# Kernel tuning notes

Measured on AMD Instinct MI355X. Metric: run time of the kernel, lower is better.

## Reference

```python
import jax, jax.numpy as jnp
import numpy as np

B, S, D, H = 8, 512, 2048, 16
DOWN, UP, R = 512, 2048, 512
HD = D // H        # 128, used only in the additive scale
VHD = UP // H      # 128, content head dim / value head dim
BASE = 10000.0


def _rope_tables(head_dim):
    # Faithful to source: positions span arange(head_dim), NOT max_len.
    pos = jnp.arange(head_dim, dtype=jnp.float32)
    div = jnp.exp(jnp.arange(0, head_dim, 2, dtype=jnp.float32) * (-np.log(BASE) / head_dim))
    theta = jnp.outer(pos, div)          # [head_dim, head_dim//2]
    return jnp.sin(theta), jnp.cos(theta)


def _apply_rope(q, num_heads, head_dim):
    # q: [B, S, num_heads*head_dim] -> [B, num_heads, S, head_dim] with interleaved rotation
    b, s, _ = q.shape
    q = q.reshape(b, s, num_heads, head_dim).transpose(0, 2, 1, 3)
    sin, cos = _rope_tables(head_dim)
    sin = sin[:s][None, None]            # [1,1,S,head_dim//2]
    cos = cos[:s][None, None]
    q_ = q.reshape(b, num_heads, s, head_dim // 2, 2)
    q1, q2 = q_[..., 0], q_[..., 1]
    o1 = q1 * cos - q2 * sin
    o2 = q2 * cos + q1 * sin
    return jnp.stack([o1, o2], axis=-1).reshape(b, num_heads, s, head_dim)


def setup_inputs() -> dict:
    key = jax.random.key(0)
    ks = jax.random.split(key, 18)
    w = lambda k, shp: jax.random.normal(k, shp, jnp.float32) * 0.02
    return {
        "X":    jax.random.normal(ks[0], (B, S, D), jnp.float32),
        "Wdq":  w(ks[1], (D, DOWN)),      "bdq":  w(ks[2], (DOWN,)),
        "Wdkv": w(ks[3], (D, DOWN)),      "bdkv": w(ks[4], (DOWN,)),
        "Wuq":  w(ks[5], (DOWN, UP)),     "buq":  w(ks[6], (UP,)),
        "Wuk":  w(ks[7], (DOWN, UP)),     "buk":  w(ks[8], (UP,)),
        "Wuv":  w(ks[9], (DOWN, UP)),     "buv":  w(ks[10], (UP,)),
        "Wqr":  w(ks[11], (DOWN, R * H)), "bqr":  w(ks[12], (R * H,)),
        "Wkr":  w(ks[13], (D, R)),        "bkr":  w(ks[14], (R,)),
        "Wfc":  w(ks[15], (VHD * H, D)),  "bfc":  w(ks[16], (D,)),
    }


def reference(X, Wdq, bdq, Wdkv, bdkv, Wuq, buq, Wuk, buk, Wuv, buv,
              Wqr, bqr, Wkr, bkr, Wfc, bfc):
    b, s, _ = X.shape
    c_q = X @ Wdq + bdq                                  # [B,S,DOWN]
    c_kv = X @ Wdkv + bdkv                               # [B,S,DOWN]
    q_c = (c_q @ Wuq + buq).reshape(b, s, H, VHD).transpose(0, 2, 1, 3)   # [B,H,S,VHD]
    k_c = (c_kv @ Wuk + buk).reshape(b, s, H, VHD).transpose(0, 2, 1, 3)
    v_c = (c_kv @ Wuv + buv).reshape(b, s, H, VHD).transpose(0, 2, 1, 3)
    q_r = _apply_rope(c_q @ Wqr + bqr, H, R)             # [B,H,S,R]
    k_r = _apply_rope(X @ Wkr + bkr, 1, R)               # [B,1,S,R]
    q = jnp.concatenate([q_c, q_r], axis=-1)             # [B,H,S,VHD+R]
    k = jnp.concatenate([k_c, jnp.broadcast_to(k_r, (b, H, s, R))], axis=-1)
    scale = HD ** 0.5 + R ** 0.5                         # additive scale, as in source
    scores = jnp.einsum('bhqd,bhkd->bhqk', q, k) / scale
    attn = jax.nn.softmax(scores, axis=-1)               # dropout: eval mode (identity)
    o = jnp.einsum('bhqk,bhkd->bhqd', attn, v_c).transpose(0, 2, 1, 3).reshape(b, s, H * VHD)
    return o @ Wfc + bfc
```

## Files before the change

### kernel.cpp

```cpp
#include <hip/hip_runtime.h>
#include <hip/hip_bf16.h>
#include <stdint.h>

typedef unsigned short u16;
typedef short bf16x8 __attribute__((ext_vector_type(8)));
typedef float f32x4 __attribute__((ext_vector_type(4)));

__device__ __forceinline__ float us2f(u16 u) {
    union { unsigned int i; float f; } x;
    x.i = ((unsigned int)u) << 16;
    return x.f;
}

__device__ __forceinline__ u16 f2us(float f) {
    union { float f; unsigned int i; } x; x.f = f;
    unsigned int lsb = (x.i >> 16) & 1u;
    x.i += 0x7FFFu + lsb;
    return (u16)(x.i >> 16);
}

__device__ __forceinline__ void gl_lds16(const u16* g, u16* l) {
    __builtin_amdgcn_global_load_lds(
        (const __attribute__((address_space(1))) void*)(uintptr_t)(const void*)g,
        (__attribute__((address_space(3))) void*)(uintptr_t)(void*)l,
        16, 0, 0);
}

#define FLAG_ROPE2  1
#define FLAG_SCALE  2
#define FLAG_TRANS2 4
#define FLAG_F32OUT 8

struct GArgs {
    const u16 *A0, *B0, *B0r2, *A1, *B1;
    long sA0o, sA0i, sB0o, sB0i, sA1o, sA1i, sB1o, sB1i;
    int K0, K1;
    const float* bias;
    void* C; void* C2; long sCo, sCi;
    int colSplit;
    int innerCnt;
    float scale;
};

template <int LDA0, int LDB0, int LDC, int LDC2, int FLAGS, int LDA1, int LDB1>
__global__ __launch_bounds__(256)
void gemm_mfma(GArgs g)
{
    __shared__ u16 As[128 * 64];
    __shared__ u16 Bs[128 * 64];

    const int t    = threadIdx.x;
    const int lane = t & 63;
    const int w    = t >> 6;
    const int wm   = w >> 1, wn = w & 1;
    const int m0   = blockIdx.y * 128;
    const int n0   = blockIdx.x * 128;
    const bool r2  = (n0 >= g.colSplit);

    const int z  = blockIdx.z;
    const int zo = z / g.innerCnt, zi = z - zo * g.innerCnt;

    const int srow = t >> 3;
    const int sp   = t & 7;
    u16* dA = As + t * 8;
    u16* dB = Bs + t * 8;

    const int lr = lane & 15;
    const int jj = lane >> 4;

    f32x4 acc[4][4];
#pragma unroll
    for (int i = 0; i < 4; ++i)
#pragma unroll
        for (int j = 0; j < 4; ++j)
            acc[i][j] = (f32x4){0.f, 0.f, 0.f, 0.f};

    auto mfma_tile = [&]() {
#pragma unroll
        for (int s = 0; s < 2; ++s) {
            bf16x8 af[4], bfr[4];
#pragma unroll
            for (int mi = 0; mi < 4; ++mi) {
                int row  = wm * 64 + mi * 16 + lr;
                int slot = (s * 4 + jj + row) & 7;
                af[mi] = *(const bf16x8*)&As[row * 64 + slot * 8];
            }
#pragma unroll
            for (int ni = 0; ni < 4; ++ni) {
                int row  = wn * 64 + ni * 16 + lr;
                int slot = (s * 4 + jj + row) & 7;
                bfr[ni] = *(const bf16x8*)&Bs[row * 64 + slot * 8];
            }
#pragma unroll
            for (int mi = 0; mi < 4; ++mi)
#pragma unroll
                for (int ni = 0; ni < 4; ++ni)
                    acc[mi][ni] = __builtin_amdgcn_mfma_f32_16x16x32_bf16(
                        af[mi], bfr[ni], acc[mi][ni], 0, 0, 0);
        }
    };

    {
        const u16* A = g.A0 + zo * g.sA0o + zi * g.sA0i;
        const u16* B = (r2 ? g.B0r2 - (long)g.colSplit * LDB0 : g.B0)
                       + zo * g.sB0o + zi * g.sB0i;
        const u16* gA[4];
        const u16* gB[4];
#pragma unroll
        for (int r = 0; r < 4; ++r) {
            int row = r * 32 + srow;
            int gc  = (sp - row) & 7;
            gA[r] = A + (long)(m0 + row) * LDA0 + gc * 8;
            gB[r] = B + (long)(n0 + row) * LDB0 + gc * 8;
        }
        for (int kt = 0; kt < g.K0; kt += 64) {
#pragma unroll
            for (int r = 0; r < 4; ++r) {
                gl_lds16(gA[r], dA + r * 2048);
                gl_lds16(gB[r], dB + r * 2048);
                gA[r] += 64; gB[r] += 64;
            }
            __syncthreads();
            mfma_tile();
            __syncthreads();
        }
    }

    if (LDA1 != 0) {
        const u16* A = g.A1 + zo * g.sA1o + zi * g.sA1i;
        const u16* B = g.B1 + zo * g.sB1o + zi * g.sB1i;
        const u16* gA[4];
        const u16* gB[4];
#pragma unroll
        for (int r = 0; r < 4; ++r) {
            int row = r * 32 + srow;
            int gc  = (sp - row) & 7;
            gA[r] = A + (long)(m0 + row) * (LDA1 ? LDA1 : 1) + gc * 8;
            gB[r] = B + (long)(n0 + row) * (LDB1 ? LDB1 : 1) + gc * 8;
        }
        for (int kt = 0; kt < g.K1; kt += 64) {
#pragma unroll
            for (int r = 0; r < 4; ++r) {
                gl_lds16(gA[r], dA + r * 2048);
                gl_lds16(gB[r], dB + r * 2048);
                gA[r] += 64; gB[r] += 64;
            }
            __syncthreads();
            mfma_tile();
            __syncthreads();
        }
    }

    const int eCol0 = n0 + wn * 64 + lr;
    const int eRow0 = m0 + wm * 64 + jj * 4;
    const bool oddc = lane & 1;

    float biasv[4];
    if (g.bias) {
#pragma unroll
        for (int ni = 0; ni < 4; ++ni) biasv[ni] = g.bias[eCol0 + ni * 16];
    }

#pragma unroll
    for (int mi = 0; mi < 4; ++mi) {
#pragma unroll
        for (int ni = 0; ni < 4; ++ni) {
            f32x4 v = acc[mi][ni];
            if (g.bias) {
                float bv = biasv[ni];
                v[0] += bv; v[1] += bv; v[2] += bv; v[3] += bv;
            }
            if (FLAGS & FLAG_SCALE) {
                v[0] *= g.scale; v[1] *= g.scale; v[2] *= g.scale; v[3] *= g.scale;
            }
            const int colg = eCol0 + ni * 16;
            const int rowb = eRow0 + mi * 16;
            if (!r2) {
                if (FLAGS & FLAG_F32OUT) {
                    float* cp = (float*)g.C + zo * g.sCo + zi * g.sCi;
#pragma unroll
                    for (int i = 0; i < 4; ++i)
                        cp[(long)(rowb + i) * LDC + colg] = v[i];
                } else {
                    u16* cp = (u16*)g.C + zo * g.sCo + zi * g.sCi;
#pragma unroll
                    for (int i = 0; i < 4; ++i)
                        cp[(long)(rowb + i) * LDC + colg] = f2us(v[i]);
                }
            } else {
                const int col2 = colg - g.colSplit;
                if (FLAGS & FLAG_ROPE2) {
                    int rp = col2 & 511 & ~1;
                    float freq = __expf(-9.2103403719761836f * (float)rp * (1.0f / 512.0f));
#pragma unroll
                    for (int i = 0; i < 4; ++i) {
                        float th = (float)((rowb + i) & 511) * freq;
                        float sn, cs;
                        __sincosf(th, &sn, &cs);
                        float other = __shfl_xor(v[i], 1, 64);
                        v[i] = oddc ? (v[i] * cs + other * sn)
                                    : (v[i] * cs - other * sn);
                    }
                }
                if (FLAGS & FLAG_TRANS2) {
                    u16* cp = (u16*)g.C2 + (long)col2 * LDC2 + rowb;
                    ushort4 o4;
                    o4.x = f2us(v[0]); o4.y = f2us(v[1]);
                    o4.z = f2us(v[2]); o4.w = f2us(v[3]);
                    *(ushort4*)cp = o4;
                } else {
                    u16* cp = (u16*)g.C2;
#pragma unroll
                    for (int i = 0; i < 4; ++i)
                        cp[(long)(rowb + i) * LDC2 + col2] = f2us(v[i]);
                }
            }
        }
    }
}

__global__ __launch_bounds__(256)
void pv_soft(const u16* __restrict__ attn, const u16* __restrict__ v_t,
             u16* __restrict__ o, int b0)
{
    __shared__ u16 Ae[32 * 512];
    __shared__ u16 Bv[128 * 64];
    __shared__ float l_arr[32];

    const int t    = threadIdx.x;
    const int lane = t & 63;
    const int w    = t >> 6;
    const int z    = blockIdx.y;
    const int bb   = b0 + (z >> 4);
    const int h    = z & 15;
    const int m0   = blockIdx.x * 32;

    const u16* Abase = attn + (long)z * 262144 + (long)m0 * 512;
#pragma unroll
    for (int i = 0; i < 8; ++i) {
        int row = w * 8 + i;
        int gc  = (lane - row) & 63;
        gl_lds16(Abase + (long)row * 512 + gc * 8, Ae + row * 512 + lane * 8);
    }
    __syncthreads();

    {
        int r = t >> 3, p = t & 7;
        u16* rp_ = Ae + r * 512;
        float mx = -1e30f;
#pragma unroll
        for (int j = 0; j < 8; ++j) {
            int slot = (p + 8 * j + r) & 63;
            bf16x8 vv = *(const bf16x8*)&rp_[slot * 8];
#pragma unroll
            for (int e = 0; e < 8; ++e) mx = fmaxf(mx, us2f(((u16*)&vv)[e]));
        }
        mx = fmaxf(mx, __shfl_xor(mx, 1, 64));
        mx = fmaxf(mx, __shfl_xor(mx, 2, 64));
        mx = fmaxf(mx, __shfl_xor(mx, 4, 64));
        float s = 0.f;
#pragma unroll
        for (int j = 0; j < 8; ++j) {
            int slot = (p + 8 * j + r) & 63;
            bf16x8 vv = *(const bf16x8*)&rp_[slot * 8];
            bf16x8 ov;
#pragma unroll
            for (int e = 0; e < 8; ++e) {
                float ee = __expf(us2f(((u16*)&vv)[e]) - mx);
                s += ee;
                ((u16*)&ov)[e] = f2us(ee);
            }
            *(bf16x8*)&rp_[slot * 8] = ov;
        }
        s += __shfl_xor(s, 1, 64);
        s += __shfl_xor(s, 2, 64);
        s += __shfl_xor(s, 4, 64);
        if (p == 0) l_arr[r] = s;
    }
    __syncthreads();

    const int lr = lane & 15;
    const int jj = lane >> 4;
    f32x4 acc[2][2];
#pragma unroll
    for (int i = 0; i < 2; ++i)
#pragma unroll
        for (int j = 0; j < 2; ++j) acc[i][j] = (f32x4){0.f, 0.f, 0.f, 0.f};

    const u16* gB[4];
    u16* dB = Bv + t * 8;
#pragma unroll
    for (int r = 0; r < 4; ++r) {
        int row = r * 32 + (t >> 3);
        int gc  = ((t & 7) - row) & 7;
        gB[r] = v_t + (long)(h * 128 + row) * 4096 + (long)bb * 512 + gc * 8;
    }
    for (int kt = 0; kt < 8; ++kt) {
#pragma unroll
        for (int r = 0; r < 4; ++r) {
            gl_lds16(gB[r], dB + r * 2048);
            gB[r] += 64;
        }
        __syncthreads();
#pragma unroll
        for (int s = 0; s < 2; ++s) {
            int kc = kt * 8 + s * 4 + jj;
            bf16x8 af[2], bfr[2];
#pragma unroll
            for (int mi = 0; mi < 2; ++mi) {
                int rowa = mi * 16 + lr;
                int slot = (kc + rowa) & 63;
                af[mi] = *(const bf16x8*)&Ae[rowa * 512 + slot * 8];
            }
#pragma unroll
            for (int ni = 0; ni < 2; ++ni) {
                int rowb = w * 32 + ni * 16 + lr;
                int slot = (s * 4 + jj + rowb) & 7;
                bfr[ni] = *(const bf16x8*)&Bv[rowb * 64 + slot * 8];
            }
#pragma unroll
            for (int mi = 0; mi < 2; ++mi)
#pragma unroll
                for (int ni = 0; ni < 2; ++ni)
                    acc[mi][ni] = __builtin_amdgcn_mfma_f32_16x16x32_bf16(
                        af[mi], bfr[ni], acc[mi][ni], 0, 0, 0);
        }
        __syncthreads();
    }

#pragma unroll
    for (int mi = 0; mi < 2; ++mi) {
#pragma unroll
        for (int i = 0; i < 4; ++i) {
            int row_l = mi * 16 + jj * 4 + i;
            float linv = 1.0f / l_arr[row_l];
            long grow = (long)(bb * 512 + m0 + row_l) * 2048 + h * 128;
#pragma unroll
            for (int ni = 0; ni < 2; ++ni) {
                int colc = w * 32 + ni * 16 + lr;
                o[grow + colc] = f2us(acc[mi][ni][i] * linv);
            }
        }
    }
}

__global__ __launch_bounds__(256)
void conv_f32_bf16(const float* __restrict__ in, u16* __restrict__ out)
{
    int i = blockIdx.x * 256 + threadIdx.x;
    float4 v = ((const float4*)in)[i];
    ushort4 o;
    o.x = f2us(v.x); o.y = f2us(v.y); o.z = f2us(v.z); o.w = f2us(v.w);
    ((ushort4*)out)[i] = o;
}

struct TC3 { const float* in0; const float* in1; const float* in2;
             u16* out; long outStride; int K; int N; };

__global__ __launch_bounds__(256)
void tconv3(TC3 a)
{
    __shared__ float tile[32][33];
    const float* in = blockIdx.z == 0 ? a.in0 : (blockIdx.z == 1 ? a.in1 : a.in2);
    u16* out = a.out + blockIdx.z * a.outStride;
    int n0 = blockIdx.x * 32, k0 = blockIdx.y * 32;
    int c = threadIdx.x & 31, r0 = threadIdx.x >> 5;
#pragma unroll
    for (int j = 0; j < 4; ++j) {
        int r = r0 + j * 8;
        tile[r][c] = in[(long)(k0 + r) * a.N + n0 + c];
    }
    __syncthreads();
#pragma unroll
    for (int j = 0; j < 4; ++j) {
        int r = r0 + j * 8;
        out[(long)(n0 + r) * a.K + k0 + c] = f2us(tile[c][r]);
    }
}

extern "C" void kernel_launch(void* const* d_in, const int* in_sizes, int n_in,
                              void* d_out, int out_size, void* d_ws, size_t ws_size,
                              hipStream_t stream)
{
    (void)in_sizes; (void)n_in; (void)out_size; (void)ws_size;

    const float* X    = (const float*)d_in[0];
    const float* Wdq  = (const float*)d_in[1];  const float* bdq  = (const float*)d_in[2];
    const float* Wdkv = (const float*)d_in[3];  const float* bdkv = (const float*)d_in[4];
    const float* Wuq  = (const float*)d_in[5];  const float* buq  = (const float*)d_in[6];
    const float* Wuk  = (const float*)d_in[7];  const float* buk  = (const float*)d_in[8];
    const float* Wuv  = (const float*)d_in[9];  const float* buv  = (const float*)d_in[10];
    const float* Wqr  = (const float*)d_in[11]; const float* bqr  = (const float*)d_in[12];
    const float* Wkr  = (const float*)d_in[13]; const float* bkr  = (const float*)d_in[14];
    const float* Wfc  = (const float*)d_in[15]; const float* bfc  = (const float*)d_in[16];
    float* out = (float*)d_out;

    u16* ws = (u16*)d_ws;
    u16* Xb     = ws;
    u16* Wc1    = Xb   + 8388608;
    u16* Wc2    = Wc1  + 3145728;
    u16* Wqr_t  = Wc2  + 3145728;
    u16* attn   = Xb;
    u16* Wfc_t  = Wqr_t + 4194304;
    u16* ckk    = Wfc_t + 4194304;
    u16* q_c    = ckk  + 6291456;
    u16* k_c    = q_c  + 8388608;
    u16* v_t    = k_c  + 8388608;
    u16* q_r    = v_t  + 8388608;
    u16* o      = q_r  + 33554432;
    float* biasD = (float*)(o + 8388608);
    float* biasQ = biasD + 1536;
    float* biasK = biasQ + 10240;

    dim3 blk(256, 1, 1);

    conv_f32_bf16<<<8192, blk, 0, stream>>>(X, Xb);
    {   TC3 a{Wdq, Wdkv, Wkr, Wc1, 1048576, 2048, 512};
        tconv3<<<dim3(16, 64, 3), blk, 0, stream>>>(a); }
    {   TC3 a{Wuq, Wuk, Wuv, Wc2, 1048576, 512, 2048};
        tconv3<<<dim3(64, 16, 3), blk, 0, stream>>>(a); }
    {   TC3 a{Wqr, nullptr, nullptr, Wqr_t, 0, 512, 8192};
        tconv3<<<dim3(256, 16, 1), blk, 0, stream>>>(a); }
    {   TC3 a{Wfc, nullptr, nullptr, Wfc_t, 0, 2048, 2048};
        tconv3<<<dim3(64, 64, 1), blk, 0, stream>>>(a); }
    hipMemcpyAsync(biasD,        bdq,  512 * 4,  hipMemcpyDeviceToDevice, stream);
    hipMemcpyAsync(biasD + 512,  bdkv, 512 * 4,  hipMemcpyDeviceToDevice, stream);
    hipMemcpyAsync(biasD + 1024, bkr,  512 * 4,  hipMemcpyDeviceToDevice, stream);
    hipMemcpyAsync(biasQ,        buq,  2048 * 4, hipMemcpyDeviceToDevice, stream);
    hipMemcpyAsync(biasQ + 2048, bqr,  8192 * 4, hipMemcpyDeviceToDevice, stream);
    hipMemcpyAsync(biasK,        buk,  2048 * 4, hipMemcpyDeviceToDevice, stream);
    hipMemcpyAsync(biasK + 2048, buv,  2048 * 4, hipMemcpyDeviceToDevice, stream);

    const int NOSPLIT = 1 << 30;

    {
        GArgs a{};
        a.A0 = Xb; a.B0 = Wc1; a.B0r2 = Wc1 + 2l * 1048576; a.K0 = 2048;
        a.bias = biasD; a.C = ckk; a.C2 = ckk + 1024;
        a.colSplit = 1024; a.innerCnt = 1; a.scale = 1.f;
        gemm_mfma<2048, 2048, 1536, 1536, FLAG_ROPE2, 0, 0>
            <<<dim3(12, 32, 1), blk, 0, stream>>>(a);
    }
    {
        GArgs a{};
        a.A0 = ckk; a.B0 = Wc2; a.B0r2 = Wqr_t; a.K0 = 512;
        a.bias = biasQ; a.C = q_c; a.C2 = q_r;
        a.colSplit = 2048; a.innerCnt = 1; a.scale = 1.f;
        gemm_mfma<1536, 512, 2048, 8192, FLAG_ROPE2, 0, 0>
            <<<dim3(80, 32, 1), blk, 0, stream>>>(a);
    }
    {
        GArgs a{};
        a.A0 = ckk + 512; a.B0 = Wc2 + 1048576; a.B0r2 = Wc2 + 2l * 1048576;
        a.K0 = 512;
        a.bias = biasK; a.C = k_c; a.C2 = v_t;
        a.colSplit = 2048; a.innerCnt = 1; a.scale = 1.f;
        gemm_mfma<1536, 512, 2048, 4096, FLAG_TRANS2, 0, 0>
            <<<dim3(32, 32, 1), blk, 0, stream>>>(a);
    }

    for (int half = 0; half < 2; ++half) {
        long b0 = half * 4;
        {
            GArgs a{};
            a.A0 = q_c + b0 * 1048576; a.sA0o = 1048576; a.sA0i = 128; a.K0 = 128;
            a.B0 = k_c + b0 * 1048576; a.sB0o = 1048576; a.sB0i = 128;
            a.B0r2 = a.B0;
            a.A1 = q_r + b0 * 4194304; a.sA1o = 4194304; a.sA1i = 512; a.K1 = 512;
            a.B1 = ckk + 1024 + b0 * 786432; a.sB1o = 786432; a.sB1i = 0;
            a.C = attn; a.C2 = attn; a.sCo = 16l * 262144; a.sCi = 262144;
            a.colSplit = NOSPLIT; a.innerCnt = 16;
            a.scale = 1.0f / 33.941125496954285f;
            gemm_mfma<2048, 2048, 512, 1, FLAG_SCALE, 8192, 1536>
                <<<dim3(4, 4, 64), blk, 0, stream>>>(a);
        }
        pv_soft<<<dim3(16, 64, 1), blk, 0, stream>>>(attn, v_t, o, (int)b0);
    }

    {
        GArgs a{};
        a.A0 = o; a.B0 = Wfc_t; a.B0r2 = Wfc_t; a.K0 = 2048;
        a.bias = bfc; a.C = out; a.C2 = out;
        a.colSplit = NOSPLIT; a.innerCnt = 1; a.scale = 1.f;
        gemm_mfma<2048, 2048, 2048, 1, FLAG_F32OUT, 0, 0>
            <<<dim3(16, 32, 1), blk, 0, stream>>>(a);
    }
}
```

Measured before the change: 481.3 us.

## Fuse QK scores, softmax and PV into one attention kernel; cheaper RoPE epilogue

```diff
diff --git a/kernel.cpp b/kernel.cpp
--- a/kernel.cpp
+++ b/kernel.cpp
@@ -27,22 +27,18 @@
 }
 
 #define FLAG_ROPE2  1
-#define FLAG_SCALE  2
 #define FLAG_TRANS2 4
 #define FLAG_F32OUT 8
 
 struct GArgs {
-    const u16 *A0, *B0, *B0r2, *A1, *B1;
-    long sA0o, sA0i, sB0o, sB0i, sA1o, sA1i, sB1o, sB1i;
-    int K0, K1;
+    const u16 *A0, *B0, *B0r2;
+    int K0;
     const float* bias;
-    void* C; void* C2; long sCo, sCi;
+    void* C; void* C2;
     int colSplit;
-    int innerCnt;
-    float scale;
 };
 
-template <int LDA0, int LDB0, int LDC, int LDC2, int FLAGS, int LDA1, int LDB1>
+template <int LDA0, int LDB0, int LDC, int LDC2, int FLAGS>
 __global__ __launch_bounds__(256)
 void gemm_mfma(GArgs g)
 {
@@ -57,9 +53,6 @@
     const int n0   = blockIdx.x * 128;
     const bool r2  = (n0 >= g.colSplit);
 
-    const int z  = blockIdx.z;
-    const int zo = z / g.innerCnt, zi = z - zo * g.innerCnt;
-
     const int srow = t >> 3;
     const int sp   = t & 7;
     u16* dA = As + t * 8;
@@ -75,35 +68,9 @@
         for (int j = 0; j < 4; ++j)
             acc[i][j] = (f32x4){0.f, 0.f, 0.f, 0.f};
 
-    auto mfma_tile = [&]() {
-#pragma unroll
-        for (int s = 0; s < 2; ++s) {
-            bf16x8 af[4], bfr[4];
-#pragma unroll
-            for (int mi = 0; mi < 4; ++mi) {
-                int row  = wm * 64 + mi * 16 + lr;
-                int slot = (s * 4 + jj + row) & 7;
-                af[mi] = *(const bf16x8*)&As[row * 64 + slot * 8];
-            }
-#pragma unroll
-            for (int ni = 0; ni < 4; ++ni) {
-                int row  = wn * 64 + ni * 16 + lr;
-                int slot = (s * 4 + jj + row) & 7;
-                bfr[ni] = *(const bf16x8*)&Bs[row * 64 + slot * 8];
-            }
-#pragma unroll
-            for (int mi = 0; mi < 4; ++mi)
-#pragma unroll
-                for (int ni = 0; ni < 4; ++ni)
-                    acc[mi][ni] = __builtin_amdgcn_mfma_f32_16x16x32_bf16(
-                        af[mi], bfr[ni], acc[mi][ni], 0, 0, 0);
-        }
-    };
-
     {
-        const u16* A = g.A0 + zo * g.sA0o + zi * g.sA0i;
-        const u16* B = (r2 ? g.B0r2 - (long)g.colSplit * LDB0 : g.B0)
-                       + zo * g.sB0o + zi * g.sB0i;
+        const u16* A = g.A0;
+        const u16* B = r2 ? g.B0r2 - (long)g.colSplit * LDB0 : g.B0;
         const u16* gA[4];
         const u16* gB[4];
 #pragma unroll
@@ -121,32 +88,28 @@
                 gA[r] += 64; gB[r] += 64;
             }
             __syncthreads();
-            mfma_tile();
-            __syncthreads();
-        }
-    }
-
-    if (LDA1 != 0) {
-        const u16* A = g.A1 + zo * g.sA1o + zi * g.sA1i;
-        const u16* B = g.B1 + zo * g.sB1o + zi * g.sB1i;
-        const u16* gA[4];
-        const u16* gB[4];
-#pragma unroll
-        for (int r = 0; r < 4; ++r) {
-            int row = r * 32 + srow;
-            int gc  = (sp - row) & 7;
-            gA[r] = A + (long)(m0 + row) * (LDA1 ? LDA1 : 1) + gc * 8;
-            gB[r] = B + (long)(n0 + row) * (LDB1 ? LDB1 : 1) + gc * 8;
-        }
-        for (int kt = 0; kt < g.K1; kt += 64) {
-#pragma unroll
-            for (int r = 0; r < 4; ++r) {
-                gl_lds16(gA[r], dA + r * 2048);
-                gl_lds16(gB[r], dB + r * 2048);
-                gA[r] += 64; gB[r] += 64;
-            }
-            __syncthreads();
-            mfma_tile();
+#pragma unroll
+            for (int s = 0; s < 2; ++s) {
+                bf16x8 af[4], bfr[4];
+#pragma unroll
+                for (int mi = 0; mi < 4; ++mi) {
+                    int row  = wm * 64 + mi * 16 + lr;
+                    int slot = (s * 4 + jj + row) & 7;
+                    af[mi] = *(const bf16x8*)&As[row * 64 + slot * 8];
+                }
+#pragma unroll
+                for (int ni = 0; ni < 4; ++ni) {
+                    int row  = wn * 64 + ni * 16 + lr;
+                    int slot = (s * 4 + jj + row) & 7;
+                    bfr[ni] = *(const bf16x8*)&Bs[row * 64 + slot * 8];
+                }
+#pragma unroll
+                for (int mi = 0; mi < 4; ++mi)
+#pragma unroll
+                    for (int ni = 0; ni < 4; ++ni)
+                        acc[mi][ni] = __builtin_amdgcn_mfma_f32_16x16x32_bf16(
+                            af[mi], bfr[ni], acc[mi][ni], 0, 0, 0);
+            }
             __syncthreads();
         }
     }
@@ -155,190 +118,270 @@
     const int eRow0 = m0 + wm * 64 + jj * 4;
     const bool oddc = lane & 1;
 
-    float biasv[4];
     if (g.bias) {
 #pragma unroll
-        for (int ni = 0; ni < 4; ++ni) biasv[ni] = g.bias[eCol0 + ni * 16];
-    }
-
-#pragma unroll
-    for (int mi = 0; mi < 4; ++mi) {
-#pragma unroll
         for (int ni = 0; ni < 4; ++ni) {
-            f32x4 v = acc[mi][ni];
-            if (g.bias) {
-                float bv = biasv[ni];
-                v[0] += bv; v[1] += bv; v[2] += bv; v[3] += bv;
-            }
-            if (FLAGS & FLAG_SCALE) {
-                v[0] *= g.scale; v[1] *= g.scale; v[2] *= g.scale; v[3] *= g.scale;
-            }
-            const int colg = eCol0 + ni * 16;
-            const int rowb = eRow0 + mi * 16;
-            if (!r2) {
+            float bv = g.bias[eCol0 + ni * 16];
+#pragma unroll
+            for (int mi = 0; mi < 4; ++mi) {
+                acc[mi][ni][0] += bv; acc[mi][ni][1] += bv;
+                acc[mi][ni][2] += bv; acc[mi][ni][3] += bv;
+            }
+        }
+    }
+
+    if (!r2) {
+#pragma unroll
+        for (int mi = 0; mi < 4; ++mi)
+#pragma unroll
+            for (int ni = 0; ni < 4; ++ni) {
+                int rowb = eRow0 + mi * 16;
+                int colg = eCol0 + ni * 16;
                 if (FLAGS & FLAG_F32OUT) {
-                    float* cp = (float*)g.C + zo * g.sCo + zi * g.sCi;
+                    float* cp = (float*)g.C;
 #pragma unroll
                     for (int i = 0; i < 4; ++i)
-                        cp[(long)(rowb + i) * LDC + colg] = v[i];
+                        cp[(long)(rowb + i) * LDC + colg] = acc[mi][ni][i];
                 } else {
-                    u16* cp = (u16*)g.C + zo * g.sCo + zi * g.sCi;
+                    u16* cp = (u16*)g.C;
 #pragma unroll
                     for (int i = 0; i < 4; ++i)
-                        cp[(long)(rowb + i) * LDC + colg] = f2us(v[i]);
-                }
-            } else {
-                const int col2 = colg - g.colSplit;
-                if (FLAGS & FLAG_ROPE2) {
-                    int rp = col2 & 511 & ~1;
-                    float freq = __expf(-9.2103403719761836f * (float)rp * (1.0f / 512.0f));
-#pragma unroll
-                    for (int i = 0; i < 4; ++i) {
-                        float th = (float)((rowb + i) & 511) * freq;
-                        float sn, cs;
-                        __sincosf(th, &sn, &cs);
-                        float other = __shfl_xor(v[i], 1, 64);
-                        v[i] = oddc ? (v[i] * cs + other * sn)
-                                    : (v[i] * cs - other * sn);
-                    }
-                }
+                        cp[(long)(rowb + i) * LDC + colg] = f2us(acc[mi][ni][i]);
+                }
+            }
+    } else if (FLAGS & FLAG_ROPE2) {
+        const float base_s = (float)(eRow0 & 511);
+#pragma unroll
+        for (int ni = 0; ni < 4; ++ni) {
+            int col2 = eCol0 + ni * 16 - g.colSplit;
+            int rp   = (col2 & 511) & ~1;
+            float f  = __expf(-9.2103403719761836f * (float)rp * (1.0f / 512.0f));
+            float s1, c1, s16, c16, sb, cb;
+            __sincosf(f, &s1, &c1);
+            __sincosf(16.0f * f, &s16, &c16);
+            __sincosf(base_s * f, &sb, &cb);
+            float cm = cb, sm = sb;
+#pragma unroll
+            for (int mi = 0; mi < 4; ++mi) {
+                f32x4 v = acc[mi][ni];
+                float cr = cm, sr = sm;
+#pragma unroll
+                for (int i = 0; i < 4; ++i) {
+                    float other = __shfl_xor(v[i], 1, 64);
+                    v[i] = oddc ? (v[i] * cr + other * sr)
+                                : (v[i] * cr - other * sr);
+                    float cn = cr * c1 - sr * s1;
+                    sr = sr * c1 + cr * s1; cr = cn;
+                }
+                int rowb = eRow0 + mi * 16;
+                u16* cp = (u16*)g.C2;
+#pragma unroll
+                for (int i = 0; i < 4; ++i)
+                    cp[(long)(rowb + i) * LDC2 + col2] = f2us(v[i]);
+                float cn = cm * c16 - sm * s16;
+                sm = sm * c16 + cm * s16; cm = cn;
+            }
+        }
+    } else {
+#pragma unroll
+        for (int mi = 0; mi < 4; ++mi)
+#pragma unroll
+            for (int ni = 0; ni < 4; ++ni) {
+                int rowb = eRow0 + mi * 16;
+                int col2 = eCol0 + ni * 16 - g.colSplit;
                 if (FLAGS & FLAG_TRANS2) {
                     u16* cp = (u16*)g.C2 + (long)col2 * LDC2 + rowb;
                     ushort4 o4;
-                    o4.x = f2us(v[0]); o4.y = f2us(v[1]);
-                    o4.z = f2us(v[2]); o4.w = f2us(v[3]);
+                    o4.x = f2us(acc[mi][ni][0]); o4.y = f2us(acc[mi][ni][1]);
+                    o4.z = f2us(acc[mi][ni][2]); o4.w = f2us(acc[mi][ni][3]);
                     *(ushort4*)cp = o4;
                 } else {
                     u16* cp = (u16*)g.C2;
 #pragma unroll
                     for (int i = 0; i < 4; ++i)
-                        cp[(long)(rowb + i) * LDC2 + col2] = f2us(v[i]);
-                }
-            }
-        }
-    }
-}
-
-__global__ __launch_bounds__(256)
-void pv_soft(const u16* __restrict__ attn, const u16* __restrict__ v_t,
-             u16* __restrict__ o, int b0)
+                        cp[(long)(rowb + i) * LDC2 + col2] = f2us(acc[mi][ni][i]);
+                }
+            }
+    }
+}
+
+__global__ __launch_bounds__(256, 2)
+void attn_fused(const u16* __restrict__ qc, const u16* __restrict__ kc,
+                const u16* __restrict__ qr, const u16* __restrict__ kr,
+                const u16* __restrict__ vt, u16* __restrict__ o)
 {
-    __shared__ u16 Ae[32 * 512];
-    __shared__ u16 Bv[128 * 64];
-    __shared__ float l_arr[32];
+    __shared__ u16 As[128 * 32];
+    __shared__ u16 Bs[128 * 32];
+    __shared__ u16 Ps[128 * 136];
+    __shared__ float l_sum[128];
 
     const int t    = threadIdx.x;
     const int lane = t & 63;
     const int w    = t >> 6;
+    const int wm   = w >> 1, wn = w & 1;
+    const int m0   = blockIdx.x * 128;
     const int z    = blockIdx.y;
-    const int bb   = b0 + (z >> 4);
-    const int h    = z & 15;
-    const int m0   = blockIdx.x * 32;
-
-    const u16* Abase = attn + (long)z * 262144 + (long)m0 * 512;
-#pragma unroll
-    for (int i = 0; i < 8; ++i) {
-        int row = w * 8 + i;
-        int gc  = (lane - row) & 63;
-        gl_lds16(Abase + (long)row * 512 + gc * 8, Ae + row * 512 + lane * 8);
-    }
-    __syncthreads();
-
-    {
-        int r = t >> 3, p = t & 7;
-        u16* rp_ = Ae + r * 512;
-        float mx = -1e30f;
-#pragma unroll
-        for (int j = 0; j < 8; ++j) {
-            int slot = (p + 8 * j + r) & 63;
-            bf16x8 vv = *(const bf16x8*)&rp_[slot * 8];
-#pragma unroll
-            for (int e = 0; e < 8; ++e) mx = fmaxf(mx, us2f(((u16*)&vv)[e]));
-        }
-        mx = fmaxf(mx, __shfl_xor(mx, 1, 64));
-        mx = fmaxf(mx, __shfl_xor(mx, 2, 64));
-        mx = fmaxf(mx, __shfl_xor(mx, 4, 64));
-        float s = 0.f;
-#pragma unroll
-        for (int j = 0; j < 8; ++j) {
-            int slot = (p + 8 * j + r) & 63;
-            bf16x8 vv = *(const bf16x8*)&rp_[slot * 8];
-            bf16x8 ov;
-#pragma unroll
-            for (int e = 0; e < 8; ++e) {
-                float ee = __expf(us2f(((u16*)&vv)[e]) - mx);
-                s += ee;
-                ((u16*)&ov)[e] = f2us(ee);
-            }
-            *(bf16x8*)&rp_[slot * 8] = ov;
-        }
-        s += __shfl_xor(s, 1, 64);
-        s += __shfl_xor(s, 2, 64);
-        s += __shfl_xor(s, 4, 64);
-        if (p == 0) l_arr[r] = s;
-    }
-    __syncthreads();
+    const int bb   = z >> 4, h = z & 15;
+
+    if (t < 128) l_sum[t] = 0.f;
+
+    const int srow = t >> 2;
+    const int sp   = t & 3;
+    u16* dA = As + t * 8;
+    u16* dB = Bs + t * 8;
+    int rrow[2], rgc[2];
+#pragma unroll
+    for (int r = 0; r < 2; ++r) {
+        rrow[r] = r * 64 + srow;
+        rgc[r]  = (sp - (rrow[r] >> 1)) & 3;
+    }
 
     const int lr = lane & 15;
     const int jj = lane >> 4;
-    f32x4 acc[2][2];
-#pragma unroll
-    for (int i = 0; i < 2; ++i)
-#pragma unroll
-        for (int j = 0; j < 2; ++j) acc[i][j] = (f32x4){0.f, 0.f, 0.f, 0.f};
-
-    const u16* gB[4];
-    u16* dB = Bv + t * 8;
-#pragma unroll
-    for (int r = 0; r < 4; ++r) {
-        int row = r * 32 + (t >> 3);
-        int gc  = ((t & 7) - row) & 7;
-        gB[r] = v_t + (long)(h * 128 + row) * 4096 + (long)bb * 512 + gc * 8;
-    }
-    for (int kt = 0; kt < 8; ++kt) {
-#pragma unroll
-        for (int r = 0; r < 4; ++r) {
-            gl_lds16(gB[r], dB + r * 2048);
-            gB[r] += 64;
-        }
-        __syncthreads();
-#pragma unroll
-        for (int s = 0; s < 2; ++s) {
-            int kc = kt * 8 + s * 4 + jj;
-            bf16x8 af[2], bfr[2];
-#pragma unroll
-            for (int mi = 0; mi < 2; ++mi) {
-                int rowa = mi * 16 + lr;
-                int slot = (kc + rowa) & 63;
-                af[mi] = *(const bf16x8*)&Ae[rowa * 512 + slot * 8];
-            }
-#pragma unroll
-            for (int ni = 0; ni < 2; ++ni) {
-                int rowb = w * 32 + ni * 16 + lr;
-                int slot = (s * 4 + jj + rowb) & 7;
-                bfr[ni] = *(const bf16x8*)&Bv[rowb * 64 + slot * 8];
-            }
-#pragma unroll
-            for (int mi = 0; mi < 2; ++mi)
-#pragma unroll
-                for (int ni = 0; ni < 2; ++ni)
-                    acc[mi][ni] = __builtin_amdgcn_mfma_f32_16x16x32_bf16(
-                        af[mi], bfr[ni], acc[mi][ni], 0, 0, 0);
-        }
-        __syncthreads();
-    }
-
-#pragma unroll
-    for (int mi = 0; mi < 2; ++mi) {
+
+    const u16* gqc[2];
+    const u16* gqr[2];
+#pragma unroll
+    for (int r = 0; r < 2; ++r) {
+        gqc[r] = qc + (long)(bb * 512 + m0 + rrow[r]) * 2048 + h * 128 + rgc[r] * 8;
+        gqr[r] = qr + (long)(bb * 512 + m0 + rrow[r]) * 8192 + h * 512 + rgc[r] * 8;
+    }
+
+    f32x4 acc_o[4][4];
+#pragma unroll
+    for (int i = 0; i < 4; ++i)
+#pragma unroll
+        for (int j = 0; j < 4; ++j) acc_o[i][j] = (f32x4){0.f, 0.f, 0.f, 0.f};
+
+    const float scale = 1.0f / 33.941125496954285f;
+
+    for (int nt = 0; nt < 4; ++nt) {
+        const int n0k = nt * 128;
+
+        f32x4 acc_s[4][4];
+#pragma unroll
+        for (int i = 0; i < 4; ++i)
+#pragma unroll
+            for (int j = 0; j < 4; ++j) acc_s[i][j] = (f32x4){0.f, 0.f, 0.f, 0.f};
+
+        const u16* pa[2];
+        const u16* pb[2];
+#pragma unroll
+        for (int r = 0; r < 2; ++r) {
+            pa[r] = gqc[r];
+            pb[r] = kc + (long)(bb * 512 + n0k + rrow[r]) * 2048 + h * 128 + rgc[r] * 8;
+        }
+        for (int seg = 0; seg < 2; ++seg) {
+            int iters = seg == 0 ? 4 : 16;
+            for (int kt = 0; kt < iters; ++kt) {
+#pragma unroll
+                for (int r = 0; r < 2; ++r) {
+                    gl_lds16(pa[r], dA + r * 2048);
+                    gl_lds16(pb[r], dB + r * 2048);
+                    pa[r] += 32; pb[r] += 32;
+                }
+                __syncthreads();
+                bf16x8 af[4], bfr[4];
+#pragma unroll
+                for (int mi = 0; mi < 4; ++mi) {
+                    int row  = wm * 64 + mi * 16 + lr;
+                    int slot = (jj + (row >> 1)) & 3;
+                    af[mi] = *(const bf16x8*)&As[row * 32 + slot * 8];
+                }
+#pragma unroll
+                for (int ni = 0; ni < 4; ++ni) {
+                    int row  = wn * 64 + ni * 16 + lr;
+                    int slot = (jj + (row >> 1)) & 3;
+                    bfr[ni] = *(const bf16x8*)&Bs[row * 32 + slot * 8];
+                }
+#pragma unroll
+                for (int mi = 0; mi < 4; ++mi)
+#pragma unroll
+                    for (int ni = 0; ni < 4; ++ni)
+                        acc_s[mi][ni] = __builtin_amdgcn_mfma_f32_16x16x32_bf16(
+                            af[mi], bfr[ni], acc_s[mi][ni], 0, 0, 0);
+                __syncthreads();
+            }
+            if (seg == 0) {
+#pragma unroll
+                for (int r = 0; r < 2; ++r) {
+                    pa[r] = gqr[r];
+                    pb[r] = kr + (long)(bb * 512 + n0k + rrow[r]) * 1536 + rgc[r] * 8;
+                }
+            }
+        }
+
+#pragma unroll
+        for (int mi = 0; mi < 4; ++mi) {
+            float rowpart[4] = {0.f, 0.f, 0.f, 0.f};
+#pragma unroll
+            for (int ni = 0; ni < 4; ++ni) {
+                f32x4 v = acc_s[mi][ni];
+                int colP = wn * 64 + ni * 16 + lr;
+#pragma unroll
+                for (int i = 0; i < 4; ++i) {
+                    float e = __expf(v[i] * scale);
+                    rowpart[i] += e;
+                    int rowP = wm * 64 + mi * 16 + jj * 4 + i;
+                    Ps[rowP * 136 + colP] = f2us(e);
+                }
+            }
+#pragma unroll
+            for (int i = 0; i < 4; ++i) {
+                float s4 = rowpart[i];
+                s4 += __shfl_xor(s4, 1, 64);
+                s4 += __shfl_xor(s4, 2, 64);
+                s4 += __shfl_xor(s4, 4, 64);
+                s4 += __shfl_xor(s4, 8, 64);
+                if ((lane & 15) == 0)
+                    atomicAdd(&l_sum[wm * 64 + mi * 16 + jj * 4 + i], s4);
+            }
+        }
+
+        const u16* pv[2];
+#pragma unroll
+        for (int r = 0; r < 2; ++r)
+            pv[r] = vt + (long)(h * 128 + rrow[r]) * 4096 + bb * 512 + n0k + rgc[r] * 8;
+        for (int kt = 0; kt < 4; ++kt) {
+#pragma unroll
+            for (int r = 0; r < 2; ++r) {
+                gl_lds16(pv[r], dB + r * 2048);
+                pv[r] += 32;
+            }
+            __syncthreads();
+            bf16x8 af[4], bfr[4];
+#pragma unroll
+            for (int mi = 0; mi < 4; ++mi) {
+                int row = wm * 64 + mi * 16 + lr;
+                af[mi] = *(const bf16x8*)&Ps[row * 136 + (kt * 4 + jj) * 8];
+            }
+#pragma unroll
+            for (int ni = 0; ni < 4; ++ni) {
+                int row  = wn * 64 + ni * 16 + lr;
+                int slot = (jj + (row >> 1)) & 3;
+                bfr[ni] = *(const bf16x8*)&Bs[row * 32 + slot * 8];
+            }
+#pragma unroll
+            for (int mi = 0; mi < 4; ++mi)
+#pragma unroll
+                for (int ni = 0; ni < 4; ++ni)
+                    acc_o[mi][ni] = __builtin_amdgcn_mfma_f32_16x16x32_bf16(
+                        af[mi], bfr[ni], acc_o[mi][ni], 0, 0, 0);
+            __syncthreads();
+        }
+    }
+
+#pragma unroll
+    for (int mi = 0; mi < 4; ++mi) {
 #pragma unroll
         for (int i = 0; i < 4; ++i) {
-            int row_l = mi * 16 + jj * 4 + i;
-            float linv = 1.0f / l_arr[row_l];
-            long grow = (long)(bb * 512 + m0 + row_l) * 2048 + h * 128;
-#pragma unroll
-            for (int ni = 0; ni < 2; ++ni) {
-                int colc = w * 32 + ni * 16 + lr;
-                o[grow + colc] = f2us(acc[mi][ni][i] * linv);
+            int row = wm * 64 + mi * 16 + jj * 4 + i;
+            float linv = 1.0f / l_sum[row];
+            long grow = (long)(bb * 512 + m0 + row) * 2048 + h * 128;
+#pragma unroll
+            for (int ni = 0; ni < 4; ++ni) {
+                int colc = wn * 64 + ni * 16 + lr;
+                o[grow + colc] = f2us(acc_o[mi][ni][i] * linv);
             }
         }
     }
@@ -400,7 +443,6 @@
     u16* Wc1    = Xb   + 8388608;
     u16* Wc2    = Wc1  + 3145728;
     u16* Wqr_t  = Wc2  + 3145728;
-    u16* attn   = Xb;
     u16* Wfc_t  = Wqr_t + 4194304;
     u16* ckk    = Wfc_t + 4194304;
     u16* q_c    = ckk  + 6291456;
@@ -437,16 +479,16 @@
         GArgs a{};
         a.A0 = Xb; a.B0 = Wc1; a.B0r2 = Wc1 + 2l * 1048576; a.K0 = 2048;
         a.bias = biasD; a.C = ckk; a.C2 = ckk + 1024;
-        a.colSplit = 1024; a.innerCnt = 1; a.scale = 1.f;
-        gemm_mfma<2048, 2048, 1536, 1536, FLAG_ROPE2, 0, 0>
+        a.colSplit = 1024;
+        gemm_mfma<2048, 2048, 1536, 1536, FLAG_ROPE2>
             <<<dim3(12, 32, 1), blk, 0, stream>>>(a);
     }
     {
         GArgs a{};
         a.A0 = ckk; a.B0 = Wc2; a.B0r2 = Wqr_t; a.K0 = 512;
         a.bias = biasQ; a.C = q_c; a.C2 = q_r;
-        a.colSplit = 2048; a.innerCnt = 1; a.scale = 1.f;
-        gemm_mfma<1536, 512, 2048, 8192, FLAG_ROPE2, 0, 0>
+        a.colSplit = 2048;
+        gemm_mfma<1536, 512, 2048, 8192, FLAG_ROPE2>
             <<<dim3(80, 32, 1), blk, 0, stream>>>(a);
     }
     {
@@ -454,35 +496,20 @@
         a.A0 = ckk + 512; a.B0 = Wc2 + 1048576; a.B0r2 = Wc2 + 2l * 1048576;
         a.K0 = 512;
         a.bias = biasK; a.C = k_c; a.C2 = v_t;
-        a.colSplit = 2048; a.innerCnt = 1; a.scale = 1.f;
-        gemm_mfma<1536, 512, 2048, 4096, FLAG_TRANS2, 0, 0>
+        a.colSplit = 2048;
+        gemm_mfma<1536, 512, 2048, 4096, FLAG_TRANS2>
             <<<dim3(32, 32, 1), blk, 0, stream>>>(a);
     }
 
-    for (int half = 0; half < 2; ++half) {
-        long b0 = half * 4;
-        {
-            GArgs a{};
-            a.A0 = q_c + b0 * 1048576; a.sA0o = 1048576; a.sA0i = 128; a.K0 = 128;
-            a.B0 = k_c + b0 * 1048576; a.sB0o = 1048576; a.sB0i = 128;
-            a.B0r2 = a.B0;
-            a.A1 = q_r + b0 * 4194304; a.sA1o = 4194304; a.sA1i = 512; a.K1 = 512;
-            a.B1 = ckk + 1024 + b0 * 786432; a.sB1o = 786432; a.sB1i = 0;
-            a.C = attn; a.C2 = attn; a.sCo = 16l * 262144; a.sCi = 262144;
-            a.colSplit = NOSPLIT; a.innerCnt = 16;
-            a.scale = 1.0f / 33.941125496954285f;
-            gemm_mfma<2048, 2048, 512, 1, FLAG_SCALE, 8192, 1536>
-                <<<dim3(4, 4, 64), blk, 0, stream>>>(a);
-        }
-        pv_soft<<<dim3(16, 64, 1), blk, 0, stream>>>(attn, v_t, o, (int)b0);
-    }
+    attn_fused<<<dim3(4, 128, 1), blk, 0, stream>>>(
+        q_c, k_c, q_r, ckk + 1024, v_t, o);
 
     {
         GArgs a{};
         a.A0 = o; a.B0 = Wfc_t; a.B0r2 = Wfc_t; a.K0 = 2048;
         a.bias = bfc; a.C = out; a.C2 = out;
-        a.colSplit = NOSPLIT; a.innerCnt = 1; a.scale = 1.f;
-        gemm_mfma<2048, 2048, 2048, 1, FLAG_F32OUT, 0, 0>
+        a.colSplit = NOSPLIT;
+        gemm_mfma<2048, 2048, 2048, 1, FLAG_F32OUT>
             <<<dim3(16, 32, 1), blk, 0, stream>>>(a);
     }
 }
```

After: 478.3 us. Within noise of the previous version (-0.6%).
